# Kernel tuning notes

Hardware: AMD Instinct MI355X
Metric: run time of the kernel (lower is better)

The kernel has to match this reference:

```python
import jax, jax.numpy as jnp
import numpy as np

B, N, VF, EF, DV, DE, LN = 64, 64, 32, 16, 128, 128, 4
EPS_INNER = 128.0  # BatchNorm1d(MAX_N, internal_d_vert): 2nd positional arg is eps (faithful to source bug)
EPS_BN = 1e-5


def gev_layer(v_in, e_in, evW, evb, eW, eb, vW, vb, relu=True):
    act = jax.nn.relu if relu else (lambda x: x)
    ev = v_in @ evW + evb                                   # [B,N,De]
    # outer_v_sum: ev.unsqueeze(1) + ev.unsqueeze(2) -> [B,N,N,De]
    e_out = act(e_in @ eW + eb + ev[:, None, :, :] + ev[:, :, None, :])
    per_v_e = e_out.sum(axis=1)                             # sum-aggregate over dim 1
    v_out = act(jnp.concatenate([per_v_e, v_in], axis=-1) @ vW + vb)
    return v_out, e_out


def bn_flat(v, g, b):
    # BatchNorm1d(N*VF) on [B, N*VF] in training mode (biased var)
    x = v.reshape(-1, N * VF)
    mu = x.mean(axis=0)
    var = x.var(axis=0)
    x = (x - mu) * jax.lax.rsqrt(var + EPS_BN) * g + b
    return x.reshape(-1, N, VF)


def bn_inner(v, g, b):
    # BatchNorm1d(MAX_N, eps=128) on [B, N, D]: channels are the N axis, stats over (B, D)
    mu = v.mean(axis=(0, 2), keepdims=True)
    var = v.var(axis=(0, 2), keepdims=True)
    return (v - mu) * jax.lax.rsqrt(var + EPS_INNER) * g[None, :, None] + b[None, :, None]


def setup_inputs() -> dict:
    key = jax.random.key(0)
    ks = jax.random.split(key, 24)
    s = 0.01  # force_lin_init with init_noise=0.01, biases zero
    nrm = lambda k, shp: jax.random.normal(k, shp, dtype=jnp.float32) * s
    inp = {
        "v": jax.random.normal(ks[0], (B, N, VF), dtype=jnp.float32),
        "e": jax.random.normal(ks[1], (B, N, N, EF), dtype=jnp.float32),
        "bn_in_g": jnp.ones((N * VF,), jnp.float32),
        "bn_in_b": jnp.zeros((N * VF,), jnp.float32),
        "g1_evW": nrm(ks[2], (VF, DE)), "g1_evb": jnp.zeros((DE,), jnp.float32),
        "g1_eW": nrm(ks[3], (EF, DE)), "g1_eb": jnp.zeros((DE,), jnp.float32),
        "g1_vW": nrm(ks[4], (VF + DE, DV)), "g1_vb": jnp.zeros((DV,), jnp.float32),
        "inn_evW": nrm(ks[5], (LN, DV, DE)), "inn_evb": jnp.zeros((LN, DE), jnp.float32),
        "inn_eW": nrm(ks[6], (LN, DE, DE)), "inn_eb": jnp.zeros((LN, DE), jnp.float32),
        "inn_vW": nrm(ks[7], (LN, DV + DE, DV)), "inn_vb": jnp.zeros((LN, DV), jnp.float32),
        "bn_g": jnp.ones((LN, N), jnp.float32),
        "bn_b": jnp.zeros((LN, N), jnp.float32),
        "g3_evW": nrm(ks[8], (DV, 1)), "g3_evb": jnp.zeros((1,), jnp.float32),
        "g3_eW": nrm(ks[9], (DE, 1)), "g3_eb": jnp.zeros((1,), jnp.float32),
        "g3_vW": nrm(ks[10], (DV + 1, 1)), "g3_vb": jnp.zeros((1,), jnp.float32),
    }
    return inp


def reference(v, e, bn_in_g, bn_in_b, g1_evW, g1_evb, g1_eW, g1_eb, g1_vW, g1_vb,
              inn_evW, inn_evb, inn_eW, inn_eb, inn_vW, inn_vb, bn_g, bn_b,
              g3_evW, g3_evb, g3_eW, g3_eb, g3_vW, g3_vb):
    v = bn_flat(v, bn_in_g, bn_in_b)
    v, e = gev_layer(v, e, g1_evW, g1_evb, g1_eW, g1_eb, g1_vW, g1_vb)
    for i in range(LN):
        v_next, e_next = gev_layer(v, e, inn_evW[i], inn_evb[i], inn_eW[i], inn_eb[i], inn_vW[i], inn_vb[i])
        v = v_next + v  # resnet
        e = e_next + e
        v = bn_inner(v, bn_g[i], bn_b[i])
    v, e = gev_layer(v, e, g3_evW, g3_evb, g3_eW, g3_eb, g3_vW, g3_vb, relu=False)
    return v, e
```

## Files before the change

### kernel.cpp

```cpp
#include <hip/hip_runtime.h>
#include <hip/hip_bf16.h>


typedef __bf16 bf16_t;
typedef __bf16 bf16x8 __attribute__((ext_vector_type(8)));
typedef __bf16 bf16x4 __attribute__((ext_vector_type(4)));
typedef float f32x4 __attribute__((ext_vector_type(4)));

__device__ __forceinline__ void bar_lgkm() {
  asm volatile("s_waitcnt lgkmcnt(0)\n\ts_barrier" ::: "memory");
}

__global__ __launch_bounds__(256) void k_prep(const float* __restrict__ vin,
    const float* __restrict__ g, const float* __restrict__ bt,
    const float* __restrict__ eW, float* __restrict__ v0,
    bf16_t* __restrict__ Wt, float* __restrict__ stats) {
  const int blk = blockIdx.x, tid = threadIdx.x;
  if (blk < 8) {
    int ch = blk * 256 + tid;
    float s = 0.f, s2 = 0.f;
    for (int b = 0; b < 64; ++b) { float x = vin[b * 2048 + ch]; s += x; s2 += x * x; }
    float mu = s * (1.f / 64.f);
    float var = s2 * (1.f / 64.f) - mu * mu;
    float sc = rsqrtf(var + 1e-5f) * g[ch];
    float bb = bt[ch];
    for (int b = 0; b < 64; ++b) {
      float x = vin[b * 2048 + ch];
      v0[b * 2048 + ch] = (x - mu) * sc + bb;
    }
  } else if (blk < 264) {
    int idx = (blk - 8) * 256 + tid;
    int l = idx >> 14, r = idx & 16383, n = r >> 7, k = r & 127;
    Wt[idx] = (bf16_t)eW[(l << 14) + (k << 7) + n];
  } else {
    for (int i = tid; i < 512; i += 256) stats[i] = 0.f;
  }
}

template <int K>
__global__ __launch_bounds__(256) void k_ev(const float* __restrict__ v_in,
    const float* __restrict__ W, const float* __restrict__ bias,
    float* __restrict__ out) {
  __shared__ float rows_s[8][K];
  const int r0 = blockIdx.x * 8;
  const int tid = threadIdx.x;
  const int c = tid & 127, h = tid >> 7;
  for (int idx = tid; idx < 8 * K; idx += 256) {
    int rr = idx / K, kk = idx % K;
    rows_s[rr][kk] = v_in[(r0 + rr) * K + kk];
  }
  __syncthreads();
  float acc[4];
  const float bv = bias[c];
#pragma unroll
  for (int r = 0; r < 4; ++r) acc[r] = bv;
  for (int k4 = 0; k4 < K; k4 += 4) {
    float w0 = W[(k4 + 0) * 128 + c], w1 = W[(k4 + 1) * 128 + c];
    float w2 = W[(k4 + 2) * 128 + c], w3 = W[(k4 + 3) * 128 + c];
#pragma unroll
    for (int r = 0; r < 4; ++r) {
      float4 x = *(const float4*)&rows_s[h * 4 + r][k4];
      acc[r] += x.x * w0 + x.y * w1 + x.z * w2 + x.w * w3;
    }
  }
#pragma unroll
  for (int r = 0; r < 4; ++r) out[(r0 + h * 4 + r) * 128 + c] = acc[r];
}

__global__ __launch_bounds__(256) void k_evbn(float* __restrict__ v,
    const float* __restrict__ stats, const float* __restrict__ g,
    const float* __restrict__ bt, const float* __restrict__ W,
    const float* __restrict__ bias, float* __restrict__ out) {
  __shared__ float rows_s[8][128];
  const int r0 = blockIdx.x * 8;
  const int tid = threadIdx.x;
  const int c = tid & 127, h = tid >> 7;
#pragma unroll
  for (int u = 0; u < 4; ++u) {
    int idx = u * 256 + tid;
    int rr = idx >> 7, k = idx & 127;
    int n = (r0 + rr) & 63;
    float mu = stats[n] * (1.f / 8192.f);
    float var = stats[64 + n] * (1.f / 8192.f) - mu * mu;
    float sc = rsqrtf(var + 128.f) * g[n];
    float x = (v[(r0 + rr) * 128 + k] - mu) * sc + bt[n];
    rows_s[rr][k] = x;
    v[(r0 + rr) * 128 + k] = x;
  }
  __syncthreads();
  float acc[4];
  const float bv = bias[c];
#pragma unroll
  for (int r = 0; r < 4; ++r) acc[r] = bv;
  for (int k4 = 0; k4 < 128; k4 += 4) {
    float w0 = W[(k4 + 0) * 128 + c], w1 = W[(k4 + 1) * 128 + c];
    float w2 = W[(k4 + 2) * 128 + c], w3 = W[(k4 + 3) * 128 + c];
#pragma unroll
    for (int r = 0; r < 4; ++r) {
      float4 x = *(const float4*)&rows_s[h * 4 + r][k4];
      acc[r] += x.x * w0 + x.y * w1 + x.z * w2 + x.w * w3;
    }
  }
#pragma unroll
  for (int r = 0; r < 4; ++r) out[(r0 + h * 4 + r) * 128 + c] = acc[r];
}

__global__ __launch_bounds__(256) void k_edge_g1(const float* __restrict__ e0,
    const float* __restrict__ eW, const float* __restrict__ eb,
    const float* __restrict__ ev, bf16_t* __restrict__ e_ws,
    float* __restrict__ pve) {
  __shared__ bf16_t A0s[2][64][40];
  __shared__ bf16_t Os[2][64][136];
  const int b = blockIdx.x >> 5, j0 = (blockIdx.x & 31) * 2;
  const int tid = threadIdx.x;
  const int lane = tid & 63, w = tid >> 6;
  const int quad = lane >> 4, l16 = lane & 15;
#pragma unroll
  for (int t = 0; t < 2; ++t) {
    int idx = tid + t * 256;
    int row = idx >> 3, off = (idx & 7) * 4;
    int jc = off >> 4, k = off & 15;
    f32x4 x = *(const f32x4*)&e0[((b * 64 + row) * 64 + j0) * 16 + off];
    bf16x4 y;
#pragma unroll
    for (int r = 0; r < 4; ++r) y[r] = (bf16_t)x[r];
    *(bf16x4*)&A0s[jc][row][k] = y;
    bf16x4 z = {(bf16_t)0.f, (bf16_t)0.f, (bf16_t)0.f, (bf16_t)0.f};
    *(bf16x4*)&A0s[jc][row][16 + k] = z;
  }
  const int c0[2] = {w * 32 + quad * 4, w * 32 + 16 + quad * 4};
  bf16x8 wf[2];
#pragma unroll
  for (int nt = 0; nt < 2; ++nt) {
    const int c = w * 32 + nt * 16 + l16;
#pragma unroll
    for (int jj = 0; jj < 8; ++jj)
      wf[nt][jj] = (quad < 2) ? (bf16_t)eW[(quad * 8 + jj) * 128 + c] : (bf16_t)0.f;
  }
  f32x4 acc[2][4][2];
  {
    f32x4 ebv[2], evj[2][2], evi[4][2];
#pragma unroll
    for (int nt = 0; nt < 2; ++nt) {
      ebv[nt] = *(const f32x4*)&eb[c0[nt]];
#pragma unroll
      for (int jc = 0; jc < 2; ++jc)
        evj[jc][nt] = *(const f32x4*)&ev[(b * 64 + j0 + jc) * 128 + c0[nt]];
#pragma unroll
      for (int mt = 0; mt < 4; ++mt)
        evi[mt][nt] = *(const f32x4*)&ev[(b * 64 + mt * 16 + l16) * 128 + c0[nt]];
    }
#pragma unroll
    for (int jc = 0; jc < 2; ++jc)
#pragma unroll
      for (int mt = 0; mt < 4; ++mt)
#pragma unroll
        for (int nt = 0; nt < 2; ++nt)
          acc[jc][mt][nt] = ebv[nt] + evj[jc][nt] + evi[mt][nt];
  }
  __syncthreads();
#pragma unroll
  for (int jc = 0; jc < 2; ++jc) {
#pragma unroll
    for (int mt = 0; mt < 4; ++mt) {
      bf16x8 ef = *(const bf16x8*)&A0s[jc][mt * 16 + l16][quad * 8];
#pragma unroll
      for (int nt = 0; nt < 2; ++nt)
        acc[jc][mt][nt] = __builtin_amdgcn_mfma_f32_16x16x32_bf16(wf[nt], ef, acc[jc][mt][nt], 0, 0, 0);
    }
  }
#pragma unroll
  for (int jc = 0; jc < 2; ++jc) {
#pragma unroll
    for (int nt = 0; nt < 2; ++nt) {
      f32x4 ps = {0.f, 0.f, 0.f, 0.f};
#pragma unroll
      for (int mt = 0; mt < 4; ++mt) {
        const int i = mt * 16 + l16;
        bf16x4 outv;
#pragma unroll
        for (int r = 0; r < 4; ++r) {
          float vv = fmaxf(acc[jc][mt][nt][r], 0.f);
          ps[r] += vv;
          outv[r] = (bf16_t)vv;
        }
        *(bf16x4*)&Os[jc][i][c0[nt]] = outv;
      }
#pragma unroll
      for (int m = 1; m <= 8; m <<= 1) {
#pragma unroll
        for (int r = 0; r < 4; ++r) ps[r] += __shfl_xor(ps[r], m);
      }
      if (l16 == 0) *(f32x4*)&pve[(b * 64 + j0 + jc) * 128 + c0[nt]] = ps;
    }
  }
  __syncthreads();
  {
    bf16_t* ebase = &e_ws[((size_t)(b * 64 + j0) * 64) * 128];
#pragma unroll
    for (int t = 0; t < 8; ++t) {
      int idx = tid + t * 256;
      *(int4*)&ebase[idx * 8] =
          *(const int4*)&Os[idx >> 10][(idx >> 4) & 63][(idx & 15) * 8];
    }
  }
}

__global__ __launch_bounds__(256) void k_vg1_ev(const float* __restrict__ pve,
    const float* __restrict__ v0, const float* __restrict__ vW,
    const float* __restrict__ vb, const float* __restrict__ evW,
    const float* __restrict__ evb, float* __restrict__ v, float* __restrict__ ev) {
  __shared__ float in_s[8][160];
  __shared__ float vr[8][128];
  const int r0 = blockIdx.x * 8;
  const int tid = threadIdx.x;
  const int c = tid & 127, h = tid >> 7;
#pragma unroll
  for (int u = 0; u < 4; ++u) {
    int idx = u * 256 + tid;
    int rr = idx >> 7, k = idx & 127;
    in_s[rr][k] = pve[(r0 + rr) * 128 + k];
  }
  {
    int rr = tid >> 5, k = tid & 31;
    in_s[rr][128 + k] = v0[(r0 + rr) * 32 + k];
  }
  __syncthreads();
  float acc[4];
  const float bv = vb[c];
#pragma unroll
  for (int r = 0; r < 4; ++r) acc[r] = bv;
  for (int k4 = 0; k4 < 160; k4 += 4) {
    float w0 = vW[(k4 + 0) * 128 + c], w1 = vW[(k4 + 1) * 128 + c];
    float w2 = vW[(k4 + 2) * 128 + c], w3 = vW[(k4 + 3) * 128 + c];
#pragma unroll
    for (int r = 0; r < 4; ++r) {
      float4 x = *(const float4*)&in_s[h * 4 + r][k4];
      acc[r] += x.x * w0 + x.y * w1 + x.z * w2 + x.w * w3;
    }
  }
#pragma unroll
  for (int r = 0; r < 4; ++r) {
    float val = fmaxf(acc[r], 0.f);
    vr[h * 4 + r][c] = val;
    v[(r0 + h * 4 + r) * 128 + c] = val;
  }
  __syncthreads();
  float acc2[4];
  const float bv2 = evb[c];
#pragma unroll
  for (int r = 0; r < 4; ++r) acc2[r] = bv2;
  for (int k4 = 0; k4 < 128; k4 += 4) {
    float w0 = evW[(k4 + 0) * 128 + c], w1 = evW[(k4 + 1) * 128 + c];
    float w2 = evW[(k4 + 2) * 128 + c], w3 = evW[(k4 + 3) * 128 + c];
#pragma unroll
    for (int r = 0; r < 4; ++r) {
      float4 x = *(const float4*)&vr[h * 4 + r][k4];
      acc2[r] += x.x * w0 + x.y * w1 + x.z * w2 + x.w * w3;
    }
  }
#pragma unroll
  for (int r = 0; r < 4; ++r) ev[(r0 + h * 4 + r) * 128 + c] = acc2[r];
}

template <bool LAST>
__global__ __launch_bounds__(256) void k_edge_inner(bf16_t* __restrict__ e_ws,
    const bf16_t* __restrict__ Wt, const float* __restrict__ eb,
    const float* __restrict__ ev, float* __restrict__ pve,
    const float* __restrict__ eW3, float* __restrict__ edt) {
  __shared__ bf16_t As[2][64][136];
  __shared__ float W3s[128];
  const int b = blockIdx.x >> 5, j0 = (blockIdx.x & 31) * 2;
  const int tid = threadIdx.x;
  const int lane = tid & 63, w = tid >> 6;
  const int quad = lane >> 4, l16 = lane & 15;
  bf16_t* ebase = &e_ws[((size_t)(b * 64 + j0) * 64) * 128];
  int4 stg[8];
#pragma unroll
  for (int t = 0; t < 8; ++t) {
    int idx = tid + t * 256;
    stg[t] = *(const int4*)&ebase[idx * 8];
  }
  if (LAST) {
    if (tid < 128) W3s[tid] = eW3[tid];
  }
  bf16x8 wf[2][4];
#pragma unroll
  for (int nt = 0; nt < 2; ++nt)
#pragma unroll
    for (int ks = 0; ks < 4; ++ks)
      wf[nt][ks] = *(const bf16x8*)&Wt[(w * 32 + nt * 16 + l16) * 128 + ks * 32 + quad * 8];
  const int c0[2] = {w * 32 + quad * 4, w * 32 + 16 + quad * 4};
  f32x4 acc[2][4][2];
  {
    f32x4 ebv[2], evj[2][2], evi[4][2];
#pragma unroll
    for (int nt = 0; nt < 2; ++nt) {
      ebv[nt] = *(const f32x4*)&eb[c0[nt]];
#pragma unroll
      for (int jc = 0; jc < 2; ++jc)
        evj[jc][nt] = *(const f32x4*)&ev[(b * 64 + j0 + jc) * 128 + c0[nt]];
#pragma unroll
      for (int mt = 0; mt < 4; ++mt)
        evi[mt][nt] = *(const f32x4*)&ev[(b * 64 + mt * 16 + l16) * 128 + c0[nt]];
    }
#pragma unroll
    for (int jc = 0; jc < 2; ++jc)
#pragma unroll
      for (int mt = 0; mt < 4; ++mt)
#pragma unroll
        for (int nt = 0; nt < 2; ++nt)
          acc[jc][mt][nt] = ebv[nt] + evj[jc][nt] + evi[mt][nt];
  }
#pragma unroll
  for (int t = 0; t < 8; ++t) {
    int idx = tid + t * 256;
    *(int4*)&As[idx >> 10][(idx >> 4) & 63][(idx & 15) * 8] = stg[t];
  }
  bar_lgkm();
#pragma unroll
  for (int ks = 0; ks < 4; ++ks) {
    bf16x8 ef[2][4];
#pragma unroll
    for (int jc = 0; jc < 2; ++jc)
#pragma unroll
      for (int mt = 0; mt < 4; ++mt)
        ef[jc][mt] = *(const bf16x8*)&As[jc][mt * 16 + l16][ks * 32 + quad * 8];
#pragma unroll
    for (int jc = 0; jc < 2; ++jc)
#pragma unroll
      for (int mt = 0; mt < 4; ++mt)
#pragma unroll
        for (int nt = 0; nt < 2; ++nt)
          acc[jc][mt][nt] = __builtin_amdgcn_mfma_f32_16x16x32_bf16(wf[nt][ks], ef[jc][mt], acc[jc][mt][nt], 0, 0, 0);
  }
  bar_lgkm();
#pragma unroll
  for (int jc = 0; jc < 2; ++jc) {
#pragma unroll
    for (int nt = 0; nt < 2; ++nt) {
      f32x4 ps = {0.f, 0.f, 0.f, 0.f};
#pragma unroll
      for (int mt = 0; mt < 4; ++mt) {
        const int i = mt * 16 + l16;
        bf16x4 eo = *(const bf16x4*)&As[jc][i][c0[nt]];
        bf16x4 outv;
#pragma unroll
        for (int r = 0; r < 4; ++r) {
          float vv = fmaxf(acc[jc][mt][nt][r], 0.f);
          ps[r] += vv;
          outv[r] = (bf16_t)(vv + (float)eo[r]);
        }
        *(bf16x4*)&As[jc][i][c0[nt]] = outv;
      }
#pragma unroll
      for (int m = 1; m <= 8; m <<= 1) {
#pragma unroll
        for (int r = 0; r < 4; ++r) ps[r] += __shfl_xor(ps[r], m);
      }
      if (l16 == 0) *(f32x4*)&pve[(b * 64 + j0 + jc) * 128 + c0[nt]] = ps;
    }
  }
  bar_lgkm();
  if (!LAST) {
#pragma unroll
    for (int t = 0; t < 8; ++t) {
      int idx = tid + t * 256;
      *(int4*)&ebase[idx * 8] =
          *(const int4*)&As[idx >> 10][(idx >> 4) & 63][(idx & 15) * 8];
    }
  } else {
    const int i = tid >> 2, q = tid & 3;
#pragma unroll
    for (int jc = 0; jc < 2; ++jc) {
      float d = 0.f;
#pragma unroll
      for (int t = 0; t < 4; ++t) {
        bf16x8 x = *(const bf16x8*)&As[jc][i][q * 32 + t * 8];
#pragma unroll
        for (int u = 0; u < 8; ++u) d += (float)x[u] * W3s[q * 32 + t * 8 + u];
      }
      d += __shfl_xor(d, 1);
      d += __shfl_xor(d, 2);
      if (q == 0) edt[(b * 64 + j0 + jc) * 64 + i] = d;
    }
  }
}

__global__ __launch_bounds__(256) void k_v_inner(const float* __restrict__ pve,
    float* __restrict__ v, const float* __restrict__ vW,
    const float* __restrict__ vb, float* __restrict__ stats) {
  __shared__ float in_s[8][256];
  __shared__ float outs[8][132];
  __shared__ float part[16][2];
  const int r0 = blockIdx.x * 8;
  const int tid = threadIdx.x;
  const int c = tid & 127, h = tid >> 7;
#pragma unroll
  for (int u = 0; u < 4; ++u) {
    int idx = u * 256 + tid;
    int rr = idx >> 7, k = idx & 127;
    in_s[rr][k] = pve[(r0 + rr) * 128 + k];
    in_s[rr][128 + k] = v[(r0 + rr) * 128 + k];
  }
  __syncthreads();
  float acc[4];
  const float bv = vb[c];
#pragma unroll
  for (int r = 0; r < 4; ++r) acc[r] = bv;
  for (int k4 = 0; k4 < 256; k4 += 4) {
    float w0 = vW[(k4 + 0) * 128 + c], w1 = vW[(k4 + 1) * 128 + c];
    float w2 = vW[(k4 + 2) * 128 + c], w3 = vW[(k4 + 3) * 128 + c];
#pragma unroll
    for (int r = 0; r < 4; ++r) {
      float4 x = *(const float4*)&in_s[h * 4 + r][k4];
      acc[r] += x.x * w0 + x.y * w1 + x.z * w2 + x.w * w3;
    }
  }
#pragma unroll
  for (int r = 0; r < 4; ++r) {
    float val = fmaxf(acc[r], 0.f) + in_s[h * 4 + r][128 + c];
    outs[h * 4 + r][c] = val;
    v[(r0 + h * 4 + r) * 128 + c] = val;
  }
  __syncthreads();
  if (tid < 16) {
    int rr = tid >> 1, half = tid & 1;
    float s = 0.f, s2 = 0.f;
    for (int k = 0; k < 64; ++k) {
      float x = outs[rr][half * 64 + k];
      s += x; s2 += x * x;
    }
    part[tid][0] = s;
    part[tid][1] = s2;
  }
  __syncthreads();
  if (tid < 8) {
    int n = (r0 + tid) & 63;
    atomicAdd(&stats[n], part[tid * 2][0] + part[tid * 2 + 1][0]);
    atomicAdd(&stats[64 + n], part[tid * 2][1] + part[tid * 2 + 1][1]);
  }
}

__global__ __launch_bounds__(256) void k_g3(const float* __restrict__ vv,
    const float* __restrict__ stats3, const float* __restrict__ g,
    const float* __restrict__ bt, const float* __restrict__ evW3,
    const float* __restrict__ evb3, const float* __restrict__ eb3,
    const float* __restrict__ edt, const float* __restrict__ vW3,
    const float* __restrict__ vb3, float* __restrict__ out_v,
    float* __restrict__ out_e) {
  __shared__ float vbn[64][132];
  __shared__ float edts[64][68];
  __shared__ float scs[64], shs[64];
  __shared__ float W3e[128];
  __shared__ float vWs[132];
  __shared__ float ev3s[64];
  __shared__ float pj[4][64];
  const int b = blockIdx.x, tid = threadIdx.x;
  if (tid < 64) {
    float mu = stats3[tid] * (1.f / 8192.f);
    float var = stats3[64 + tid] * (1.f / 8192.f) - mu * mu;
    float sc = rsqrtf(var + 128.f) * g[tid];
    scs[tid] = sc;
    shs[tid] = bt[tid] - mu * sc;
  }
  if (tid < 128) W3e[tid] = evW3[tid];
  if (tid < 129) vWs[tid] = vW3[tid];
  __syncthreads();
#pragma unroll
  for (int t = 0; t < 8; ++t) {
    int idx = t * 1024 + tid * 4;
    int row = idx >> 7, cc = idx & 127;
    f32x4 x = *(const f32x4*)&vv[(b * 64 + row) * 128 + cc];
    *(f32x4*)&vbn[row][cc] = x * scs[row] + shs[row];
  }
#pragma unroll
  for (int t = 0; t < 4; ++t) {
    int idx = t * 1024 + tid * 4;
    int j = idx >> 6, i = idx & 63;
    *(f32x4*)&edts[j][i] = *(const f32x4*)&edt[(b * 64 + j) * 64 + i];
  }
  __syncthreads();
  {
    int i = tid >> 2, q = tid & 3;
    float d = 0.f;
#pragma unroll
    for (int u = 0; u < 32; ++u) d += vbn[i][q * 32 + u] * W3e[q * 32 + u];
    d += __shfl_xor(d, 1);
    d += __shfl_xor(d, 2);
    if (q == 0) ev3s[i] = d + evb3[0];
  }
  __syncthreads();
  {
    int q = tid >> 6, j = tid & 63;
    float s = 0.f;
    const float e3 = eb3[0];
    const float evj = ev3s[j];
#pragma unroll
    for (int r = 0; r < 16; ++r) {
      int i = q * 16 + r;
      float val = edts[j][i] + e3 + ev3s[i] + evj;
      out_e[(b * 64 + i) * 64 + j] = val;
      s += val;
    }
    pj[q][j] = s;
  }
  __syncthreads();
  {
    int n = tid >> 2, q = tid & 3;
    float d = 0.f;
#pragma unroll
    for (int u = 0; u < 32; ++u) d += vbn[n][q * 32 + u] * vWs[1 + q * 32 + u];
    d += __shfl_xor(d, 1);
    d += __shfl_xor(d, 2);
    if (q == 0) {
      float p3 = pj[0][n] + pj[1][n] + pj[2][n] + pj[3][n];
      out_v[b * 64 + n] = d + p3 * vWs[0] + vb3[0];
    }
  }
}

extern "C" void kernel_launch(void* const* d_in, const int* in_sizes, int n_in,
                              void* d_out, int out_size, void* d_ws, size_t ws_size,
                              hipStream_t stream) {
  const float* in_v    = (const float*)d_in[0];
  const float* in_e    = (const float*)d_in[1];
  const float* bn_in_g = (const float*)d_in[2];
  const float* bn_in_b = (const float*)d_in[3];
  const float* g1_evW  = (const float*)d_in[4];
  const float* g1_evb  = (const float*)d_in[5];
  const float* g1_eW   = (const float*)d_in[6];
  const float* g1_eb   = (const float*)d_in[7];
  const float* g1_vW   = (const float*)d_in[8];
  const float* g1_vb   = (const float*)d_in[9];
  const float* inn_evW = (const float*)d_in[10];
  const float* inn_evb = (const float*)d_in[11];
  const float* inn_eW  = (const float*)d_in[12];
  const float* inn_eb  = (const float*)d_in[13];
  const float* inn_vW  = (const float*)d_in[14];
  const float* inn_vb  = (const float*)d_in[15];
  const float* bn_g    = (const float*)d_in[16];
  const float* bn_b    = (const float*)d_in[17];
  const float* g3_evW  = (const float*)d_in[18];
  const float* g3_evb  = (const float*)d_in[19];
  const float* g3_eW   = (const float*)d_in[20];
  const float* g3_eb   = (const float*)d_in[21];
  const float* g3_vW   = (const float*)d_in[22];
  const float* g3_vb   = (const float*)d_in[23];

  char* ws = (char*)d_ws;
  bf16_t* e_ws = (bf16_t*)(ws);
  float* v     = (float*)(ws + 67108864);
  float* ev    = (float*)(ws + 69206016);
  float* pve   = (float*)(ws + 71303168);
  float* v0    = (float*)(ws + 73400320);
  bf16_t* Wt   = (bf16_t*)(ws + 73924608);
  float* edt   = (float*)(ws + 74055680);
  float* stats = (float*)(ws + 75104256);

  float* out_v = (float*)d_out;
  float* out_e = (float*)d_out + 4096;

  k_prep<<<265, 256, 0, stream>>>(in_v, bn_in_g, bn_in_b, inn_eW, v0, Wt, stats);

  k_ev<32><<<512, 256, 0, stream>>>(v0, g1_evW, g1_evb, ev);
  k_edge_g1<<<2048, 256, 0, stream>>>(in_e, g1_eW, g1_eb, ev, e_ws, pve);
  k_vg1_ev<<<512, 256, 0, stream>>>(pve, v0, g1_vW, g1_vb, inn_evW, inn_evb, v, ev);

  for (int l = 0; l < 4; ++l) {
    if (l > 0)
      k_evbn<<<512, 256, 0, stream>>>(v, stats + (l - 1) * 128, bn_g + (l - 1) * 64,
                                      bn_b + (l - 1) * 64, inn_evW + l * 16384,
                                      inn_evb + l * 128, ev);
    if (l < 3)
      k_edge_inner<false><<<2048, 256, 0, stream>>>(e_ws, Wt + l * 16384,
          inn_eb + l * 128, ev, pve, g3_eW, edt);
    else
      k_edge_inner<true><<<2048, 256, 0, stream>>>(e_ws, Wt + l * 16384,
          inn_eb + l * 128, ev, pve, g3_eW, edt);
    k_v_inner<<<512, 256, 0, stream>>>(pve, v, inn_vW + l * 32768, inn_vb + l * 128,
                                       stats + l * 128);
  }

  k_g3<<<64, 256, 0, stream>>>(v, stats + 384, bn_g + 192, bn_b + 192,
                               g3_evW, g3_evb, g3_eb, edt, g3_vW, g3_vb,
                               out_v, out_e);
}
```

Baseline: 367.7 us.

## Use direct global-to-LDS loads with XOR swizzle and finer-grained vertex kernels

```diff
diff --git a/kernel.cpp b/kernel.cpp
--- a/kernel.cpp
+++ b/kernel.cpp
@@ -9,6 +9,17 @@
 
 __device__ __forceinline__ void bar_lgkm() {
   asm volatile("s_waitcnt lgkmcnt(0)\n\ts_barrier" ::: "memory");
+}
+__device__ __forceinline__ void bar_vm() {
+  asm volatile("s_waitcnt vmcnt(0)\n\ts_barrier" ::: "memory");
+}
+
+__device__ __forceinline__ int swz(int lin) { return lin ^ (((lin >> 8) & 7) << 4); }
+
+__device__ __forceinline__ void gload_lds16(const void* g, void* l) {
+  __builtin_amdgcn_global_load_lds(
+      (const __attribute__((address_space(1))) void*)g,
+      (__attribute__((address_space(3))) void*)l, 16, 0, 0);
 }
 
 __global__ __launch_bounds__(256) void k_prep(const float* __restrict__ vin,
@@ -41,42 +52,41 @@
 __global__ __launch_bounds__(256) void k_ev(const float* __restrict__ v_in,
     const float* __restrict__ W, const float* __restrict__ bias,
     float* __restrict__ out) {
-  __shared__ float rows_s[8][K];
-  const int r0 = blockIdx.x * 8;
+  __shared__ float rows_s[4][K];
+  const int r0 = blockIdx.x * 4;
   const int tid = threadIdx.x;
   const int c = tid & 127, h = tid >> 7;
-  for (int idx = tid; idx < 8 * K; idx += 256) {
+  for (int idx = tid; idx < 4 * K; idx += 256) {
     int rr = idx / K, kk = idx % K;
     rows_s[rr][kk] = v_in[(r0 + rr) * K + kk];
   }
   __syncthreads();
-  float acc[4];
+  float acc[2];
   const float bv = bias[c];
-#pragma unroll
-  for (int r = 0; r < 4; ++r) acc[r] = bv;
+  acc[0] = bv; acc[1] = bv;
   for (int k4 = 0; k4 < K; k4 += 4) {
     float w0 = W[(k4 + 0) * 128 + c], w1 = W[(k4 + 1) * 128 + c];
     float w2 = W[(k4 + 2) * 128 + c], w3 = W[(k4 + 3) * 128 + c];
 #pragma unroll
-    for (int r = 0; r < 4; ++r) {
-      float4 x = *(const float4*)&rows_s[h * 4 + r][k4];
+    for (int r = 0; r < 2; ++r) {
+      float4 x = *(const float4*)&rows_s[h * 2 + r][k4];
       acc[r] += x.x * w0 + x.y * w1 + x.z * w2 + x.w * w3;
     }
   }
 #pragma unroll
-  for (int r = 0; r < 4; ++r) out[(r0 + h * 4 + r) * 128 + c] = acc[r];
+  for (int r = 0; r < 2; ++r) out[(r0 + h * 2 + r) * 128 + c] = acc[r];
 }
 
 __global__ __launch_bounds__(256) void k_evbn(float* __restrict__ v,
     const float* __restrict__ stats, const float* __restrict__ g,
     const float* __restrict__ bt, const float* __restrict__ W,
     const float* __restrict__ bias, float* __restrict__ out) {
-  __shared__ float rows_s[8][128];
-  const int r0 = blockIdx.x * 8;
+  __shared__ float rows_s[4][128];
+  const int r0 = blockIdx.x * 4;
   const int tid = threadIdx.x;
   const int c = tid & 127, h = tid >> 7;
 #pragma unroll
-  for (int u = 0; u < 4; ++u) {
+  for (int u = 0; u < 2; ++u) {
     int idx = u * 256 + tid;
     int rr = idx >> 7, k = idx & 127;
     int n = (r0 + rr) & 63;
@@ -88,21 +98,20 @@
     v[(r0 + rr) * 128 + k] = x;
   }
   __syncthreads();
-  float acc[4];
+  float acc[2];
   const float bv = bias[c];
-#pragma unroll
-  for (int r = 0; r < 4; ++r) acc[r] = bv;
+  acc[0] = bv; acc[1] = bv;
   for (int k4 = 0; k4 < 128; k4 += 4) {
     float w0 = W[(k4 + 0) * 128 + c], w1 = W[(k4 + 1) * 128 + c];
     float w2 = W[(k4 + 2) * 128 + c], w3 = W[(k4 + 3) * 128 + c];
 #pragma unroll
-    for (int r = 0; r < 4; ++r) {
-      float4 x = *(const float4*)&rows_s[h * 4 + r][k4];
+    for (int r = 0; r < 2; ++r) {
+      float4 x = *(const float4*)&rows_s[h * 2 + r][k4];
       acc[r] += x.x * w0 + x.y * w1 + x.z * w2 + x.w * w3;
     }
   }
 #pragma unroll
-  for (int r = 0; r < 4; ++r) out[(r0 + h * 4 + r) * 128 + c] = acc[r];
+  for (int r = 0; r < 2; ++r) out[(r0 + h * 2 + r) * 128 + c] = acc[r];
 }
 
 __global__ __launch_bounds__(256) void k_edge_g1(const float* __restrict__ e0,
@@ -110,7 +119,7 @@
     const float* __restrict__ ev, bf16_t* __restrict__ e_ws,
     float* __restrict__ pve) {
   __shared__ bf16_t A0s[2][64][40];
-  __shared__ bf16_t Os[2][64][136];
+  __shared__ __align__(16) bf16_t Os[2 * 64 * 128];
   const int b = blockIdx.x >> 5, j0 = (blockIdx.x & 31) * 2;
   const int tid = threadIdx.x;
   const int lane = tid & 63, w = tid >> 6;
@@ -184,7 +193,7 @@
           ps[r] += vv;
           outv[r] = (bf16_t)vv;
         }
-        *(bf16x4*)&Os[jc][i][c0[nt]] = outv;
+        *(bf16x4*)((char*)Os + swz(((jc * 64 + i) << 8) | (c0[nt] << 1))) = outv;
       }
 #pragma unroll
       for (int m = 1; m <= 8; m <<= 1) {
@@ -199,9 +208,8 @@
     bf16_t* ebase = &e_ws[((size_t)(b * 64 + j0) * 64) * 128];
 #pragma unroll
     for (int t = 0; t < 8; ++t) {
-      int idx = tid + t * 256;
-      *(int4*)&ebase[idx * 8] =
-          *(const int4*)&Os[idx >> 10][(idx >> 4) & 63][(idx & 15) * 8];
+      int off = (t * 256 + tid) * 16;
+      *(int4*)((char*)ebase + off) = *(const int4*)((const char*)Os + off);
     }
   }
 }
@@ -210,57 +218,55 @@
     const float* __restrict__ v0, const float* __restrict__ vW,
     const float* __restrict__ vb, const float* __restrict__ evW,
     const float* __restrict__ evb, float* __restrict__ v, float* __restrict__ ev) {
-  __shared__ float in_s[8][160];
-  __shared__ float vr[8][128];
-  const int r0 = blockIdx.x * 8;
+  __shared__ float in_s[4][160];
+  __shared__ float vr[4][128];
+  const int r0 = blockIdx.x * 4;
   const int tid = threadIdx.x;
   const int c = tid & 127, h = tid >> 7;
 #pragma unroll
-  for (int u = 0; u < 4; ++u) {
+  for (int u = 0; u < 2; ++u) {
     int idx = u * 256 + tid;
     int rr = idx >> 7, k = idx & 127;
     in_s[rr][k] = pve[(r0 + rr) * 128 + k];
   }
-  {
+  if (tid < 128) {
     int rr = tid >> 5, k = tid & 31;
     in_s[rr][128 + k] = v0[(r0 + rr) * 32 + k];
   }
   __syncthreads();
-  float acc[4];
+  float acc[2];
   const float bv = vb[c];
-#pragma unroll
-  for (int r = 0; r < 4; ++r) acc[r] = bv;
+  acc[0] = bv; acc[1] = bv;
   for (int k4 = 0; k4 < 160; k4 += 4) {
     float w0 = vW[(k4 + 0) * 128 + c], w1 = vW[(k4 + 1) * 128 + c];
     float w2 = vW[(k4 + 2) * 128 + c], w3 = vW[(k4 + 3) * 128 + c];
 #pragma unroll
-    for (int r = 0; r < 4; ++r) {
-      float4 x = *(const float4*)&in_s[h * 4 + r][k4];
+    for (int r = 0; r < 2; ++r) {
+      float4 x = *(const float4*)&in_s[h * 2 + r][k4];
       acc[r] += x.x * w0 + x.y * w1 + x.z * w2 + x.w * w3;
     }
   }
 #pragma unroll
-  for (int r = 0; r < 4; ++r) {
+  for (int r = 0; r < 2; ++r) {
     float val = fmaxf(acc[r], 0.f);
-    vr[h * 4 + r][c] = val;
-    v[(r0 + h * 4 + r) * 128 + c] = val;
-  }
-  __syncthreads();
-  float acc2[4];
+    vr[h * 2 + r][c] = val;
+    v[(r0 + h * 2 + r) * 128 + c] = val;
+  }
+  __syncthreads();
+  float acc2[2];
   const float bv2 = evb[c];
-#pragma unroll
-  for (int r = 0; r < 4; ++r) acc2[r] = bv2;
+  acc2[0] = bv2; acc2[1] = bv2;
   for (int k4 = 0; k4 < 128; k4 += 4) {
     float w0 = evW[(k4 + 0) * 128 + c], w1 = evW[(k4 + 1) * 128 + c];
     float w2 = evW[(k4 + 2) * 128 + c], w3 = evW[(k4 + 3) * 128 + c];
 #pragma unroll
-    for (int r = 0; r < 4; ++r) {
-      float4 x = *(const float4*)&vr[h * 4 + r][k4];
+    for (int r = 0; r < 2; ++r) {
+      float4 x = *(const float4*)&vr[h * 2 + r][k4];
       acc2[r] += x.x * w0 + x.y * w1 + x.z * w2 + x.w * w3;
     }
   }
 #pragma unroll
-  for (int r = 0; r < 4; ++r) ev[(r0 + h * 4 + r) * 128 + c] = acc2[r];
+  for (int r = 0; r < 2; ++r) ev[(r0 + h * 2 + r) * 128 + c] = acc2[r];
 }
 
 template <bool LAST>
@@ -268,18 +274,19 @@
     const bf16_t* __restrict__ Wt, const float* __restrict__ eb,
     const float* __restrict__ ev, float* __restrict__ pve,
     const float* __restrict__ eW3, float* __restrict__ edt) {
-  __shared__ bf16_t As[2][64][136];
+  __shared__ __align__(16) bf16_t As[2 * 64 * 128];
   __shared__ float W3s[128];
   const int b = blockIdx.x >> 5, j0 = (blockIdx.x & 31) * 2;
   const int tid = threadIdx.x;
   const int lane = tid & 63, w = tid >> 6;
   const int quad = lane >> 4, l16 = lane & 15;
   bf16_t* ebase = &e_ws[((size_t)(b * 64 + j0) * 64) * 128];
-  int4 stg[8];
-#pragma unroll
-  for (int t = 0; t < 8; ++t) {
-    int idx = tid + t * 256;
-    stg[t] = *(const int4*)&ebase[idx * 8];
+  {
+    const char* gsrc = (const char*)ebase;
+    char* ldst = (char*)As;
+#pragma unroll
+    for (int t = 0; t < 8; ++t)
+      gload_lds16(gsrc + (t * 256 + tid) * 16, ldst + (t * 256 + w * 64) * 16);
   }
   if (LAST) {
     if (tid < 128) W3s[tid] = eW3[tid];
@@ -312,12 +319,7 @@
         for (int nt = 0; nt < 2; ++nt)
           acc[jc][mt][nt] = ebv[nt] + evj[jc][nt] + evi[mt][nt];
   }
-#pragma unroll
-  for (int t = 0; t < 8; ++t) {
-    int idx = tid + t * 256;
-    *(int4*)&As[idx >> 10][(idx >> 4) & 63][(idx & 15) * 8] = stg[t];
-  }
-  bar_lgkm();
+  bar_vm();
 #pragma unroll
   for (int ks = 0; ks < 4; ++ks) {
     bf16x8 ef[2][4];
@@ -325,7 +327,8 @@
     for (int jc = 0; jc < 2; ++jc)
 #pragma unroll
       for (int mt = 0; mt < 4; ++mt)
-        ef[jc][mt] = *(const bf16x8*)&As[jc][mt * 16 + l16][ks * 32 + quad * 8];
+        ef[jc][mt] = *(const bf16x8*)((const char*)As +
+            swz(((jc * 64 + mt * 16 + l16) << 8) | ((ks * 32 + quad * 8) << 1)));
 #pragma unroll
     for (int jc = 0; jc < 2; ++jc)
 #pragma unroll
@@ -343,7 +346,8 @@
 #pragma unroll
       for (int mt = 0; mt < 4; ++mt) {
         const int i = mt * 16 + l16;
-        bf16x4 eo = *(const bf16x4*)&As[jc][i][c0[nt]];
+        char* cell = (char*)As + swz(((jc * 64 + i) << 8) | (c0[nt] << 1));
+        bf16x4 eo = *(const bf16x4*)cell;
         bf16x4 outv;
 #pragma unroll
         for (int r = 0; r < 4; ++r) {
@@ -351,7 +355,7 @@
           ps[r] += vv;
           outv[r] = (bf16_t)(vv + (float)eo[r]);
         }
-        *(bf16x4*)&As[jc][i][c0[nt]] = outv;
+        *(bf16x4*)cell = outv;
       }
 #pragma unroll
       for (int m = 1; m <= 8; m <<= 1) {
@@ -365,9 +369,8 @@
   if (!LAST) {
 #pragma unroll
     for (int t = 0; t < 8; ++t) {
-      int idx = tid + t * 256;
-      *(int4*)&ebase[idx * 8] =
-          *(const int4*)&As[idx >> 10][(idx >> 4) & 63][(idx & 15) * 8];
+      int off = (t * 256 + tid) * 16;
+      *(int4*)((char*)ebase + off) = *(const int4*)((const char*)As + off);
     }
   } else {
     const int i = tid >> 2, q = tid & 3;
@@ -376,7 +379,8 @@
       float d = 0.f;
 #pragma unroll
       for (int t = 0; t < 4; ++t) {
-        bf16x8 x = *(const bf16x8*)&As[jc][i][q * 32 + t * 8];
+        bf16x8 x = *(const bf16x8*)((const char*)As +
+            swz(((jc * 64 + i) << 8) | ((q * 32 + t * 8) << 1)));
 #pragma unroll
         for (int u = 0; u < 8; ++u) d += (float)x[u] * W3s[q * 32 + t * 8 + u];
       }
@@ -390,41 +394,40 @@
 __global__ __launch_bounds__(256) void k_v_inner(const float* __restrict__ pve,
     float* __restrict__ v, const float* __restrict__ vW,
     const float* __restrict__ vb, float* __restrict__ stats) {
-  __shared__ float in_s[8][256];
-  __shared__ float outs[8][132];
-  __shared__ float part[16][2];
-  const int r0 = blockIdx.x * 8;
+  __shared__ float in_s[4][256];
+  __shared__ float outs[4][132];
+  __shared__ float part[8][2];
+  const int r0 = blockIdx.x * 4;
   const int tid = threadIdx.x;
   const int c = tid & 127, h = tid >> 7;
 #pragma unroll
-  for (int u = 0; u < 4; ++u) {
+  for (int u = 0; u < 2; ++u) {
     int idx = u * 256 + tid;
     int rr = idx >> 7, k = idx & 127;
     in_s[rr][k] = pve[(r0 + rr) * 128 + k];
     in_s[rr][128 + k] = v[(r0 + rr) * 128 + k];
   }
   __syncthreads();
-  float acc[4];
+  float acc[2];
   const float bv = vb[c];
-#pragma unroll
-  for (int r = 0; r < 4; ++r) acc[r] = bv;
+  acc[0] = bv; acc[1] = bv;
   for (int k4 = 0; k4 < 256; k4 += 4) {
     float w0 = vW[(k4 + 0) * 128 + c], w1 = vW[(k4 + 1) * 128 + c];
     float w2 = vW[(k4 + 2) * 128 + c], w3 = vW[(k4 + 3) * 128 + c];
 #pragma unroll
-    for (int r = 0; r < 4; ++r) {
-      float4 x = *(const float4*)&in_s[h * 4 + r][k4];
+    for (int r = 0; r < 2; ++r) {
+      float4 x = *(const float4*)&in_s[h * 2 + r][k4];
       acc[r] += x.x * w0 + x.y * w1 + x.z * w2 + x.w * w3;
     }
   }
 #pragma unroll
-  for (int r = 0; r < 4; ++r) {
-    float val = fmaxf(acc[r], 0.f) + in_s[h * 4 + r][128 + c];
-    outs[h * 4 + r][c] = val;
-    v[(r0 + h * 4 + r) * 128 + c] = val;
-  }
-  __syncthreads();
-  if (tid < 16) {
+  for (int r = 0; r < 2; ++r) {
+    float val = fmaxf(acc[r], 0.f) + in_s[h * 2 + r][128 + c];
+    outs[h * 2 + r][c] = val;
+    v[(r0 + h * 2 + r) * 128 + c] = val;
+  }
+  __syncthreads();
+  if (tid < 8) {
     int rr = tid >> 1, half = tid & 1;
     float s = 0.f, s2 = 0.f;
     for (int k = 0; k < 64; ++k) {
@@ -435,14 +438,14 @@
     part[tid][1] = s2;
   }
   __syncthreads();
-  if (tid < 8) {
+  if (tid < 4) {
     int n = (r0 + tid) & 63;
     atomicAdd(&stats[n], part[tid * 2][0] + part[tid * 2 + 1][0]);
     atomicAdd(&stats[64 + n], part[tid * 2][1] + part[tid * 2 + 1][1]);
   }
 }
 
-__global__ __launch_bounds__(256) void k_g3(const float* __restrict__ vv,
+__global__ __launch_bounds__(1024) void k_g3(const float* __restrict__ vv,
     const float* __restrict__ stats3, const float* __restrict__ g,
     const float* __restrict__ bt, const float* __restrict__ evW3,
     const float* __restrict__ evb3, const float* __restrict__ eb3,
@@ -455,7 +458,7 @@
   __shared__ float W3e[128];
   __shared__ float vWs[132];
   __shared__ float ev3s[64];
-  __shared__ float pj[4][64];
+  __shared__ float pj[16][64];
   const int b = blockIdx.x, tid = threadIdx.x;
   if (tid < 64) {
     float mu = stats3[tid] * (1.f / 8192.f);
@@ -468,26 +471,27 @@
   if (tid < 129) vWs[tid] = vW3[tid];
   __syncthreads();
 #pragma unroll
-  for (int t = 0; t < 8; ++t) {
-    int idx = t * 1024 + tid * 4;
+  for (int t = 0; t < 2; ++t) {
+    int idx = t * 4096 + tid * 4;
     int row = idx >> 7, cc = idx & 127;
     f32x4 x = *(const f32x4*)&vv[(b * 64 + row) * 128 + cc];
     *(f32x4*)&vbn[row][cc] = x * scs[row] + shs[row];
   }
-#pragma unroll
-  for (int t = 0; t < 4; ++t) {
-    int idx = t * 1024 + tid * 4;
+  {
+    int idx = tid * 4;
     int j = idx >> 6, i = idx & 63;
     *(f32x4*)&edts[j][i] = *(const f32x4*)&edt[(b * 64 + j) * 64 + i];
   }
   __syncthreads();
   {
-    int i = tid >> 2, q = tid & 3;
+    int i = tid >> 4, q = tid & 15;
     float d = 0.f;
 #pragma unroll
-    for (int u = 0; u < 32; ++u) d += vbn[i][q * 32 + u] * W3e[q * 32 + u];
+    for (int u = 0; u < 8; ++u) d += vbn[i][q * 8 + u] * W3e[q * 8 + u];
     d += __shfl_xor(d, 1);
     d += __shfl_xor(d, 2);
+    d += __shfl_xor(d, 4);
+    d += __shfl_xor(d, 8);
     if (q == 0) ev3s[i] = d + evb3[0];
   }
   __syncthreads();
@@ -497,8 +501,8 @@
     const float e3 = eb3[0];
     const float evj = ev3s[j];
 #pragma unroll
-    for (int r = 0; r < 16; ++r) {
-      int i = q * 16 + r;
+    for (int r = 0; r < 4; ++r) {
+      int i = q * 4 + r;
       float val = edts[j][i] + e3 + ev3s[i] + evj;
       out_e[(b * 64 + i) * 64 + j] = val;
       s += val;
@@ -507,14 +511,18 @@
   }
   __syncthreads();
   {
-    int n = tid >> 2, q = tid & 3;
+    int n = tid >> 4, q = tid & 15;
     float d = 0.f;
 #pragma unroll
-    for (int u = 0; u < 32; ++u) d += vbn[n][q * 32 + u] * vWs[1 + q * 32 + u];
+    for (int u = 0; u < 8; ++u) d += vbn[n][q * 8 + u] * vWs[1 + q * 8 + u];
     d += __shfl_xor(d, 1);
     d += __shfl_xor(d, 2);
+    d += __shfl_xor(d, 4);
+    d += __shfl_xor(d, 8);
     if (q == 0) {
-      float p3 = pj[0][n] + pj[1][n] + pj[2][n] + pj[3][n];
+      float p3 = 0.f;
+#pragma unroll
+      for (int qq = 0; qq < 16; ++qq) p3 += pj[qq][n];
       out_v[b * 64 + n] = d + p3 * vWs[0] + vb3[0];
     }
   }
@@ -563,26 +571,26 @@
 
   k_prep<<<265, 256, 0, stream>>>(in_v, bn_in_g, bn_in_b, inn_eW, v0, Wt, stats);
 
-  k_ev<32><<<512, 256, 0, stream>>>(v0, g1_evW, g1_evb, ev);
+  k_ev<32><<<1024, 256, 0, stream>>>(v0, g1_evW, g1_evb, ev);
   k_edge_g1<<<2048, 256, 0, stream>>>(in_e, g1_eW, g1_eb, ev, e_ws, pve);
-  k_vg1_ev<<<512, 256, 0, stream>>>(pve, v0, g1_vW, g1_vb, inn_evW, inn_evb, v, ev);
+  k_vg1_ev<<<1024, 256, 0, stream>>>(pve, v0, g1_vW, g1_vb, inn_evW, inn_evb, v, ev);
 
   for (int l = 0; l < 4; ++l) {
     if (l > 0)
-      k_evbn<<<512, 256, 0, stream>>>(v, stats + (l - 1) * 128, bn_g + (l - 1) * 64,
-                                      bn_b + (l - 1) * 64, inn_evW + l * 16384,
-                                      inn_evb + l * 128, ev);
+      k_evbn<<<1024, 256, 0, stream>>>(v, stats + (l - 1) * 128, bn_g + (l - 1) * 64,
+                                       bn_b + (l - 1) * 64, inn_evW + l * 16384,
+                                       inn_evb + l * 128, ev);
     if (l < 3)
       k_edge_inner<false><<<2048, 256, 0, stream>>>(e_ws, Wt + l * 16384,
           inn_eb + l * 128, ev, pve, g3_eW, edt);
     else
       k_edge_inner<true><<<2048, 256, 0, stream>>>(e_ws, Wt + l * 16384,
           inn_eb + l * 128, ev, pve, g3_eW, edt);
-    k_v_inner<<<512, 256, 0, stream>>>(pve, v, inn_vW + l * 32768, inn_vb + l * 128,
-                                       stats + l * 128);
-  }
-
-  k_g3<<<64, 256, 0, stream>>>(v, stats + 384, bn_g + 192, bn_b + 192,
-                               g3_evW, g3_evb, g3_eb, edt, g3_vW, g3_vb,
-                               out_v, out_e);
-}
+    k_v_inner<<<1024, 256, 0, stream>>>(pve, v, inn_vW + l * 32768, inn_vb + l * 128,
+                                        stats + l * 128);
+  }
+
+  k_g3<<<64, 1024, 0, stream>>>(v, stats + 384, bn_g + 192, bn_b + 192,
+                                g3_evW, g3_evb, g3_eb, edt, g3_vW, g3_vb,
+                                out_v, out_e);
+}
```

Measured after the change: 406.8 us. 10.6% more time.
